# Performance work log

Hardware: AMD Instinct MI355X
Metric: run time of the kernel (lower is better)

Reference implementation:

```python
import jax, jax.numpy as jnp
import numpy as np

N = 20000        # nodes
E = 160000       # directed edges (before self loops)
NODE_DIM = 1287
HEADS = 4
C1, C2, C3 = 128, 256, 128
ACT_SLOPE = 0.15   # module's LeakyReLU between layers
GAT_SLOPE = 0.2    # PyG GATConv default negative_slope


def _gat_layer(x, src, dst, W, att_src, att_dst, bias, heads, out_dim, concat):
    # x: [N, in] ; W: [in, heads*out] ; att_*: [heads, out] ; bias: [heads*out] or [out]
    h = (x @ W).reshape(N, heads, out_dim)                      # [N, H, C]
    a_s = jnp.einsum('nhc,hc->nh', h, att_src)                  # [N, H]
    a_d = jnp.einsum('nhc,hc->nh', h, att_dst)                  # [N, H]
    e = jax.nn.leaky_relu(a_s[src] + a_d[dst], GAT_SLOPE)       # [Etot, H]
    # segment softmax over incoming edges of each dst node (self loops => no empty segments)
    m = jax.ops.segment_max(e, dst, num_segments=N)             # [N, H]
    w = jnp.exp(e - m[dst])
    den = jax.ops.segment_sum(w, dst, num_segments=N)           # [N, H]
    alpha = w / den[dst]                                        # [Etot, H]
    msg = h[src] * alpha[:, :, None]                            # [Etot, H, C]
    out = jax.ops.segment_sum(msg, dst, num_segments=N)         # [N, H, C]
    out = out.reshape(N, heads * out_dim) if concat else out.mean(axis=1)
    return out + bias


def setup_inputs() -> dict:
    key = jax.random.key(0)
    ks = jax.random.split(key, 22)
    s = 0.05
    x = jax.random.normal(ks[0], (N, NODE_DIM), jnp.float32)
    edge_index = jax.random.randint(ks[1], (2, E), 0, N, dtype=jnp.int64)
    inp = {
        'x': x, 'edge_index': edge_index,
        'W1': jax.random.normal(ks[2], (NODE_DIM, HEADS * C1), jnp.float32) * s,
        'as1': jax.random.normal(ks[3], (HEADS, C1), jnp.float32) * s,
        'ad1': jax.random.normal(ks[4], (HEADS, C1), jnp.float32) * s,
        'b1': jnp.zeros((HEADS * C1,), jnp.float32),
        'W2': jax.random.normal(ks[5], (HEADS * C1, HEADS * C2), jnp.float32) * s,
        'as2': jax.random.normal(ks[6], (HEADS, C2), jnp.float32) * s,
        'ad2': jax.random.normal(ks[7], (HEADS, C2), jnp.float32) * s,
        'b2': jnp.zeros((HEADS * C2,), jnp.float32),
        # conv3: 1024 -> 128, 1 head, no concat
        'W3': jax.random.normal(ks[8], (HEADS * C2, C3), jnp.float32) * s,
        'as3': jax.random.normal(ks[9], (1, C3), jnp.float32) * s,
        'ad3': jax.random.normal(ks[10], (1, C3), jnp.float32) * s,
        'b3': jnp.zeros((C3,), jnp.float32),
        # pre_fc: 128 -> 16
        'pw': jax.random.normal(ks[11], (C3, 16), jnp.float32) * s,
        'pb': jnp.zeros((16,), jnp.float32),
        # fc fallback: Linear(16,32) -> LeakyReLU(0.15) -> Linear(32,2)
        'f1w': jax.random.normal(ks[12], (16, 32), jnp.float32) * s,
        'f1b': jnp.zeros((32,), jnp.float32),
        'f2w': jax.random.normal(ks[13], (32, 2), jnp.float32) * s,
        'f2b': jnp.zeros((2,), jnp.float32),
    }
    return inp


def reference(x, edge_index, W1, as1, ad1, b1, W2, as2, ad2, b2,
              W3, as3, ad3, b3, pw, pb, f1w, f1b, f2w, f2b):
    loop = jnp.arange(N, dtype=edge_index.dtype)
    src = jnp.concatenate([edge_index[0], loop])   # PyG add_self_loops=True
    dst = jnp.concatenate([edge_index[1], loop])
    h = _gat_layer(x, src, dst, W1, as1, ad1, b1, HEADS, C1, True)
    h = jax.nn.leaky_relu(h, ACT_SLOPE)            # dropout = identity (eval)
    h = _gat_layer(h, src, dst, W2, as2, ad2, b2, HEADS, C2, True)
    h = jax.nn.leaky_relu(h, ACT_SLOPE)
    h = _gat_layer(h, src, dst, W3, as3, ad3, b3, 1, C3, False)
    h = jax.nn.leaky_relu(h, ACT_SLOPE)
    h = h @ pw + pb                                 # pre_fc (128 -> 16)
    h = jax.nn.leaky_relu(h @ f1w + f1b, ACT_SLOPE)
    return h @ f2w + f2b                            # [N, 2] logits
```

## Files before the change

### kernel.cpp

```cpp
#include <hip/hip_runtime.h>
#include <hip/hip_bf16.h>
#include <cstdint>
#include <cstddef>

#define LRELU(x, s) ((x) > 0.f ? (x) : (s) * (x))

typedef __attribute__((ext_vector_type(8))) short bf16x8;
typedef __attribute__((ext_vector_type(4))) float f32x4;

__device__ __forceinline__ float bflo(uint v) { return __uint_as_float(v << 16); }
__device__ __forceinline__ float bfhi(uint v) { return __uint_as_float(v & 0xffff0000u); }
__device__ __forceinline__ ushort f2bf(float f) {
  const uint u = __float_as_uint(f);
  return (ushort)((u + 0x7fffu + ((u >> 16) & 1u)) >> 16);
}
__device__ __forceinline__ float rl_f(float x, int j) {
  return __uint_as_float(__builtin_amdgcn_readlane(__float_as_uint(x), j));
}

__device__ __forceinline__ void async16(const ushort* g, ushort* l) {
  __builtin_amdgcn_global_load_lds(
      (const __attribute__((address_space(1))) unsigned int*)g,
      (__attribute__((address_space(3))) unsigned int*)l, 16, 0, 0);
}

#define WAITCNT_VM(n) (0xF70 | (n))

__global__ __launch_bounds__(256) void prep_all(
    const float* __restrict__ x, ushort* __restrict__ xb,
    const float* __restrict__ W1, ushort* __restrict__ W1t,
    const float* __restrict__ W2, ushort* __restrict__ W2t,
    const float* __restrict__ W3, ushort* __restrict__ W3t,
    const int* __restrict__ edst, int* __restrict__ deg, int E,
    int N, int K1, int K1p, int nA, int nB, int nC, int nD) {
  __shared__ float tile[32][33];
  const int tid = threadIdx.x;
  int b = blockIdx.x;
  if (b < nA) {
    const int P8 = K1p >> 3;
    const long long idx = (long long)b * 256 + tid;
    if (idx < (long long)N * P8) {
      const int r = (int)(idx / P8);
      const int c = ((int)(idx - (long long)r * P8)) << 3;
      const float* p = x + (size_t)r * K1 + c;
      float v[8];
      if (c + 7 < K1) {
        const float4 a = *(const float4*)p;
        const float4 bq = *(const float4*)(p + 4);
        v[0] = a.x; v[1] = a.y; v[2] = a.z; v[3] = a.w;
        v[4] = bq.x; v[5] = bq.y; v[6] = bq.z; v[7] = bq.w;
      } else {
#pragma unroll
        for (int j = 0; j < 8; j++) v[j] = (c + j < K1) ? p[j] : 0.f;
      }
      uint4 o;
      o.x = (uint)f2bf(v[0]) | ((uint)f2bf(v[1]) << 16);
      o.y = (uint)f2bf(v[2]) | ((uint)f2bf(v[3]) << 16);
      o.z = (uint)f2bf(v[4]) | ((uint)f2bf(v[5]) << 16);
      o.w = (uint)f2bf(v[6]) | ((uint)f2bf(v[7]) << 16);
      *(uint4*)(xb + (size_t)r * K1p + c) = o;
    }
    return;
  }
  b -= nA;
  if (b < nB + nC + nD) {
    const float* W; ushort* Wt; int K, Nn, Kp, tilesK;
    if (b < nB)           { W = W1; Wt = W1t; K = K1;   Nn = 512;  Kp = K1p;  tilesK = K1p / 32; }
    else if (b < nB + nC) { b -= nB; W = W2; Wt = W2t; K = 512;  Nn = 1024; Kp = 512;  tilesK = 16; }
    else                  { b -= nB + nC; W = W3; Wt = W3t; K = 1024; Nn = 128; Kp = 1024; tilesK = 32; }
    const int kt = (b % tilesK) * 32;
    const int nt = (b / tilesK) * 32;
    const int tx = tid & 31, ty = tid >> 5;
    for (int r = ty; r < 32; r += 8) {
      const int k = kt + r, nn = nt + tx;
      tile[r][tx] = (k < K && nn < Nn) ? W[(size_t)k * Nn + nn] : 0.f;
    }
    __syncthreads();
    for (int r = ty; r < 32; r += 8) {
      const int nn = nt + r, k = kt + tx;
      if (nn < Nn && k < Kp) Wt[(size_t)nn * Kp + k] = f2bf(tile[tx][r]);
    }
    return;
  }
  b -= nB + nC + nD;
  {
    const int t = b * 256 + tid;
    if (t < E) atomicAdd(&deg[edst[t]], 1);
  }
}

template <int TM, int TAG, bool BUF3>
__global__ __launch_bounds__(256) void gemm_bf16(
    const ushort* __restrict__ A, const ushort* __restrict__ Bt, ushort* __restrict__ C,
    int M, int N, int Kp, int gemmBlocks,
    const int* __restrict__ esrc, const int* __restrict__ edst, int E, int Etot,
    int* __restrict__ cursor, int* __restrict__ csr_src) {
  constexpr int MI = TM / 32;
  constexpr int LPG = (TM == 128) ? 4 : 3;
  constexpr int NBUF = BUF3 ? 3 : 2;
  __shared__ ushort sA[NBUF * TM * 32];
  __shared__ ushort sB[NBUF * 128 * 32];
  const int tid = threadIdx.x;
  const int wave = tid >> 6;
  const int lane = tid & 63;

  if (blockIdx.x >= gemmBlocks) {
    const int t = (blockIdx.x - gemmBlocks) * 256 + tid;
    if (t >= Etot) return;
    int s, d;
    if (t < E) { s = esrc[t]; d = edst[t]; } else { s = t - E; d = s; }
    const int pos = atomicAdd(&cursor[d], 1);
    csr_src[pos] = s;
    return;
  }

  const int tilesN = N >> 7;
  const int nwg = gemmBlocks;
  const int q8 = nwg >> 3, r8 = nwg & 7;
  const int xcd = blockIdx.x & 7;
  const int lid = blockIdx.x >> 3;
  const int wg = (xcd < r8 ? xcd * (q8 + 1) : r8 * (q8 + 1) + (xcd - r8) * q8) + lid;
  const int bx = wg % tilesN;
  const int by = wg / tilesN;
  const int wrow = (wave >> 1) * (TM / 2);
  const int wcol = (wave & 1) * 64;
  const int quad = lane >> 4;
  const int ml = lane & 15;

  const int seg = (((lane & 3) ^ ((lane >> 3) & 3)) * 8);
  const int rB0 = wave * 32 + (lane >> 2);
  const int gB0 = bx * 128 + rB0;
  const ushort* pB0 = Bt + (size_t)gB0 * Kp + seg;
  const ushort* pB1 = Bt + (size_t)(gB0 + 16) * Kp + seg;
  ushort* lB0 = &sB[(wave * 32) * 32];
  ushort* lB1 = &sB[(wave * 32 + 16) * 32];
  const ushort *pA0, *pA1;
  ushort *lA0, *lA1;
  if constexpr (TM == 128) {
    const int r0 = wave * 32 + (lane >> 2);
    pA0 = A + (size_t)min(by * TM + r0, M - 1) * Kp + seg;
    pA1 = A + (size_t)min(by * TM + r0 + 16, M - 1) * Kp + seg;
    lA0 = &sA[(wave * 32) * 32];
    lA1 = &sA[(wave * 32 + 16) * 32];
  } else {
    const int r0 = wave * 16 + (lane >> 2);
    pA0 = A + (size_t)min(by * TM + r0, M - 1) * Kp + seg;
    pA1 = nullptr;
    lA0 = &sA[(wave * 16) * 32];
    lA1 = nullptr;
  }

  const int nIter = Kp >> 5;
  auto issue = [&](int it, int p) {
    const int k0 = it << 5;
    const int oa = p * TM * 32;
    const int ob_ = p * 128 * 32;
    async16(pA0 + k0, lA0 + oa);
    if constexpr (TM == 128) async16(pA1 + k0, lA1 + oa);
    async16(pB0 + k0, lB0 + ob_);
    async16(pB1 + k0, lB1 + ob_);
  };

  f32x4 acc[MI][4];
#pragma unroll
  for (int mi = 0; mi < MI; mi++)
#pragma unroll
    for (int ni = 0; ni < 4; ni++)
#pragma unroll
      for (int e = 0; e < 4; e++) acc[mi][ni][e] = 0.f;

  const int rq = (quad ^ ((ml >> 1) & 3)) * 8;

  issue(0, 0);
  if (nIter > 1) issue(1, 1);
  int b = 0;
  for (int it = 0; it < nIter; ++it) {
    if (it + 1 < nIter) __builtin_amdgcn_s_waitcnt(WAITCNT_VM(LPG));
    else __builtin_amdgcn_s_waitcnt(WAITCNT_VM(0));
    __builtin_amdgcn_s_barrier();
    if constexpr (BUF3) {
      if (it + 2 < nIter) {
        const int b2 = (b + 2 >= 3) ? b - 1 : b + 2;
        issue(it + 2, b2);
      }
    }
    const ushort* bA = &sA[b * TM * 32];
    const ushort* bB = &sB[b * 128 * 32];
    bf16x8 af[MI], bfr[4];
#pragma unroll
    for (int mi = 0; mi < MI; mi++)
      af[mi] = *(const bf16x8*)&bA[(wrow + mi * 16 + ml) * 32 + rq];
#pragma unroll
    for (int ni = 0; ni < 4; ni++)
      bfr[ni] = *(const bf16x8*)&bB[(wcol + ni * 16 + ml) * 32 + rq];
#pragma unroll
    for (int mi = 0; mi < MI; mi++)
#pragma unroll
      for (int ni = 0; ni < 4; ni++)
        acc[mi][ni] = __builtin_amdgcn_mfma_f32_16x16x32_bf16(af[mi], bfr[ni], acc[mi][ni], 0, 0, 0);
    if constexpr (!BUF3) {
      if (it + 2 < nIter) {
        __builtin_amdgcn_s_barrier();
        issue(it + 2, b);
      }
      b ^= 1;
    } else {
      b = (b + 1 == 3) ? 0 : b + 1;
    }
  }

#pragma unroll
  for (int mi = 0; mi < MI; mi++) {
#pragma unroll
    for (int r = 0; r < 4; r++) {
      const int row = by * TM + wrow + mi * 16 + quad * 4 + r;
      if (row < M) {
#pragma unroll
        for (int ni = 0; ni < 4; ni++) {
          const int col = bx * 128 + wcol + ni * 16 + ml;
          C[(size_t)row * N + col] = f2bf(acc[mi][ni][r]);
        }
      }
    }
  }
}

template <int H, int C>
__global__ __launch_bounds__(256) void att_dots(
    const ushort* __restrict__ hb, const float* __restrict__ AS,
    const float* __restrict__ AD, float* __restrict__ asb, float* __restrict__ adb,
    int Nn) {
  constexpr int HC = H * C;
  constexpr int EPL = HC / 64;
  constexpr int S = C / EPL;
  const int n = blockIdx.x * 4 + (threadIdx.x >> 6);
  const int lane = threadIdx.x & 63;
  if (n >= Nn) return;
  const int head = lane / S;
  const int cbase = (lane % S) * EPL;
  const ushort* row = hb + (size_t)n * HC + lane * EPL;
  const float* as_h = AS + head * C;
  const float* ad_h = AD + head * C;
  float ps = 0.f, pd = 0.f;
#pragma unroll
  for (int j = 0; j < EPL; j += 2) {
    const uint v = *(const uint*)(row + j);
    const float lo = bflo(v), hi = bfhi(v);
    ps += lo * as_h[cbase + j] + hi * as_h[cbase + j + 1];
    pd += lo * ad_h[cbase + j] + hi * ad_h[cbase + j + 1];
  }
#pragma unroll
  for (int off = 1; off < S; off <<= 1) {
    ps += __shfl_xor(ps, off);
    pd += __shfl_xor(pd, off);
  }
  if ((lane % S) == 0) {
    asb[n * H + head] = ps;
    adb[n * H + head] = pd;
  }
}

__global__ __launch_bounds__(1024) void scan_kernel(const int* __restrict__ deg,
                                                    int* __restrict__ rowptr,
                                                    int* __restrict__ cursor, int n) {
  __shared__ int swsum[16];
  __shared__ int carry_s;
  const int t = threadIdx.x;
  const int wv = t >> 6, lane = t & 63;
  if (t == 0) carry_s = 0;
  __syncthreads();
  for (int base = 0; base < n; base += 1024) {
    const int i = base + t;
    const int v = (i < n) ? (deg[i] + 1) : 0;
    int sc = v;
#pragma unroll
    for (int off = 1; off < 64; off <<= 1) {
      const int u = __shfl_up(sc, off);
      if (lane >= off) sc += u;
    }
    if (lane == 63) swsum[wv] = sc;
    __syncthreads();
    if (t < 16) {
      int x = swsum[t];
#pragma unroll
      for (int off = 1; off < 16; off <<= 1) {
        const int u = __shfl_up(x, off);
        if (t >= off) x += u;
      }
      swsum[t] = x;
    }
    __syncthreads();
    const int incl = sc + (wv == 0 ? 0 : swsum[wv - 1]) + carry_s;
    if (i < n) { rowptr[i + 1] = incl; cursor[i] = incl - v; }
    if (base == 0 && t == 0) rowptr[0] = 0;
    __syncthreads();
    if (t == 0) carry_s += swsum[15];
    __syncthreads();
  }
}

template <int H, int C>
__global__ __launch_bounds__(256) void gat_agg_wave(
    const ushort* __restrict__ hb, const int* __restrict__ rowptr,
    const int* __restrict__ csr_src, const float* __restrict__ a_s,
    const float* __restrict__ a_d, const float* __restrict__ bias,
    ushort* __restrict__ outb, float act_slope, int Nn) {
  constexpr int HC = H * C;
  constexpr int NU = HC / 2;
  constexpr int UPT = NU / 256;
  constexpr int GRP = (UPT == 2) ? 4 : 8;
  const int n = blockIdx.x * 4 + (threadIdx.x >> 6);
  const int lane = threadIdx.x & 63;
  if (n >= Nn) return;
  float ad_n[H];
#pragma unroll
  for (int h = 0; h < H; h++) ad_n[h] = a_d[n * H + h];
  const int start = rowptr[n], end = rowptr[n + 1];
  f32x4 acc[UPT][2];
#pragma unroll
  for (int q = 0; q < UPT; q++)
#pragma unroll
    for (int u = 0; u < 2; u++)
#pragma unroll
      for (int e = 0; e < 4; e++) acc[q][u][e] = 0.f;
  float den[H];
#pragma unroll
  for (int h = 0; h < H; h++) den[h] = 0.f;

  for (int base = start; base < end; base += 64) {
    const int cnt = min(64, end - base);
    int s = 0;
    float w[H];
#pragma unroll
    for (int h = 0; h < H; h++) w[h] = 0.f;
    if (lane < cnt) {
      s = csr_src[base + lane];
      float asv[H];
      if constexpr (H == 4) {
        const float4 t4 = *(const float4*)(a_s + s * 4);
        asv[0] = t4.x; asv[1] = t4.y; asv[2] = t4.z; asv[3] = t4.w;
      } else {
        asv[0] = a_s[s];
      }
#pragma unroll
      for (int h = 0; h < H; h++) {
        float lg = asv[h] + ad_n[h];
        lg = LRELU(lg, 0.2f);
        w[h] = __expf(lg);
        den[h] += w[h];
      }
    }
    const int cntg = cnt & ~(GRP - 1);
    int j = 0;
    for (; j < cntg; j += GRP) {
      uint4 v[GRP][UPT];
#pragma unroll
      for (int g = 0; g < GRP; g++) {
        const int sj = __builtin_amdgcn_readlane(s, j + g);
        const uint4* hp = (const uint4*)(hb + (size_t)sj * HC);
#pragma unroll
        for (int q = 0; q < UPT; q++) v[g][q] = hp[q * 64 + lane];
      }
#pragma unroll
      for (int g = 0; g < GRP; g++) {
        float wj[H];
#pragma unroll
        for (int h = 0; h < H; h++) wj[h] = rl_f(w[h], j + g);
#pragma unroll
        for (int q = 0; q < UPT; q++) {
          const int e0 = q * 512 + 8 * lane;
          const float wq = wj[e0 / C];
          acc[q][0][0] += wq * bflo(v[g][q].x);
          acc[q][0][1] += wq * bfhi(v[g][q].x);
          acc[q][0][2] += wq * bflo(v[g][q].y);
          acc[q][0][3] += wq * bfhi(v[g][q].y);
          acc[q][1][0] += wq * bflo(v[g][q].z);
          acc[q][1][1] += wq * bfhi(v[g][q].z);
          acc[q][1][2] += wq * bflo(v[g][q].w);
          acc[q][1][3] += wq * bfhi(v[g][q].w);
        }
      }
    }
    for (; j < cnt; j++) {
      const int sj = __builtin_amdgcn_readlane(s, j);
      float wj[H];
#pragma unroll
      for (int h = 0; h < H; h++) wj[h] = rl_f(w[h], j);
      const uint4* hp = (const uint4*)(hb + (size_t)sj * HC);
#pragma unroll
      for (int q = 0; q < UPT; q++) {
        const int e0 = q * 512 + 8 * lane;
        const uint4 v = hp[q * 64 + lane];
        const float wq = wj[e0 / C];
        acc[q][0][0] += wq * bflo(v.x);
        acc[q][0][1] += wq * bfhi(v.x);
        acc[q][0][2] += wq * bflo(v.y);
        acc[q][0][3] += wq * bfhi(v.y);
        acc[q][1][0] += wq * bflo(v.z);
        acc[q][1][1] += wq * bfhi(v.z);
        acc[q][1][2] += wq * bflo(v.w);
        acc[q][1][3] += wq * bfhi(v.w);
      }
    }
  }
#pragma unroll
  for (int h = 0; h < H; h++) {
#pragma unroll
    for (int off = 1; off < 64; off <<= 1) den[h] += __shfl_xor(den[h], off);
    den[h] = 1.f / den[h];
  }
#pragma unroll
  for (int q = 0; q < UPT; q++) {
    const int e0 = q * 512 + 8 * lane;
    const float iv = den[e0 / C];
    const float4 ba = *(const float4*)(bias + e0);
    const float4 bb = *(const float4*)(bias + e0 + 4);
    const float o0 = LRELU(acc[q][0][0] * iv + ba.x, act_slope);
    const float o1 = LRELU(acc[q][0][1] * iv + ba.y, act_slope);
    const float o2 = LRELU(acc[q][0][2] * iv + ba.z, act_slope);
    const float o3 = LRELU(acc[q][0][3] * iv + ba.w, act_slope);
    const float o4 = LRELU(acc[q][1][0] * iv + bb.x, act_slope);
    const float o5 = LRELU(acc[q][1][1] * iv + bb.y, act_slope);
    const float o6 = LRELU(acc[q][1][2] * iv + bb.z, act_slope);
    const float o7 = LRELU(acc[q][1][3] * iv + bb.w, act_slope);
    uint4 o;
    o.x = (uint)f2bf(o0) | ((uint)f2bf(o1) << 16);
    o.y = (uint)f2bf(o2) | ((uint)f2bf(o3) << 16);
    o.z = (uint)f2bf(o4) | ((uint)f2bf(o5) << 16);
    o.w = (uint)f2bf(o6) | ((uint)f2bf(o7) << 16);
    ((uint4*)outb)[(size_t)n * (NU / 4) + q * 64 + lane] = o;
  }
}

__global__ __launch_bounds__(256) void gat_agg3_mlp(
    const ushort* __restrict__ hb, const int* __restrict__ rowptr,
    const int* __restrict__ csr_src, const float* __restrict__ a_s,
    const float* __restrict__ a_d, const float* __restrict__ b3,
    const float* __restrict__ pw, const float* __restrict__ pb,
    const float* __restrict__ f1w, const float* __restrict__ f1b,
    const float* __restrict__ f2w, const float* __restrict__ f2b,
    float* __restrict__ out, int Nn) {
  __shared__ float sx[4][128];
  __shared__ float s1[4][16];
  __shared__ float s2[4][32];
  const int w = threadIdx.x >> 6;
  const int lane = threadIdx.x & 63;
  const int n = blockIdx.x * 4 + w;
  if (n >= Nn) return;
  const float ad_n = a_d[n];
  const int start = rowptr[n], end = rowptr[n + 1];
  float2 acc = make_float2(0.f, 0.f);
  float den = 0.f;
  for (int base = start; base < end; base += 64) {
    const int cnt = min(64, end - base);
    int s = 0;
    float wv_ = 0.f;
    if (lane < cnt) {
      s = csr_src[base + lane];
      float lg = a_s[s] + ad_n;
      lg = LRELU(lg, 0.2f);
      wv_ = __expf(lg);
      den += wv_;
    }
    const int cntg = cnt & ~7;
    int j = 0;
    for (; j < cntg; j += 8) {
      uint v[8];
      float wj[8];
#pragma unroll
      for (int g = 0; g < 8; g++) {
        const int sj = __builtin_amdgcn_readlane(s, j + g);
        v[g] = ((const uint*)(hb + (size_t)sj * 128))[lane];
        wj[g] = rl_f(wv_, j + g);
      }
#pragma unroll
      for (int g = 0; g < 8; g++) {
        acc.x += wj[g] * bflo(v[g]);
        acc.y += wj[g] * bfhi(v[g]);
      }
    }
    for (; j < cnt; j++) {
      const int sj = __builtin_amdgcn_readlane(s, j);
      const float wj = rl_f(wv_, j);
      const uint v = ((const uint*)(hb + (size_t)sj * 128))[lane];
      acc.x += wj * bflo(v);
      acc.y += wj * bfhi(v);
    }
  }
#pragma unroll
  for (int off = 1; off < 64; off <<= 1) den += __shfl_xor(den, off);
  const float iv = 1.f / den;
  sx[w][2 * lane]     = LRELU(acc.x * iv + b3[2 * lane], 0.15f);
  sx[w][2 * lane + 1] = LRELU(acc.y * iv + b3[2 * lane + 1], 0.15f);
  {
    const int o = lane & 15, p = lane >> 4;
    float a = 0.f;
#pragma unroll
    for (int c = 0; c < 32; c++) a += sx[w][p * 32 + c] * pw[(p * 32 + c) * 16 + o];
    a += __shfl_xor(a, 16);
    a += __shfl_xor(a, 32);
    if (lane < 16) s1[w][o] = a + pb[o];
  }
  {
    const int o = lane & 31, p = lane >> 5;
    float a = 0.f;
#pragma unroll
    for (int c = 0; c < 8; c++) a += s1[w][p * 8 + c] * f1w[(p * 8 + c) * 32 + o];
    a += __shfl_xor(a, 32);
    if (lane < 32) s2[w][o] = LRELU(a + f1b[o], 0.15f);
  }
  {
    const int o = lane & 1, p = lane >> 1;
    float a = s2[w][p] * f2w[p * 2 + o];
    a += __shfl_xor(a, 2);
    a += __shfl_xor(a, 4);
    a += __shfl_xor(a, 8);
    a += __shfl_xor(a, 16);
    a += __shfl_xor(a, 32);
    if (lane < 2) out[(size_t)n * 2 + o] = a + f2b[o];
  }
}

extern "C" void kernel_launch(void* const* d_in, const int* in_sizes, int n_in,
                              void* d_out, int out_size, void* d_ws, size_t ws_size,
                              hipStream_t stream) {
  const float* x   = (const float*)d_in[0];
  const int* ei    = (const int*)d_in[1];
  const float* W1  = (const float*)d_in[2];
  const float* as1 = (const float*)d_in[3];
  const float* ad1 = (const float*)d_in[4];
  const float* b1  = (const float*)d_in[5];
  const float* W2  = (const float*)d_in[6];
  const float* as2 = (const float*)d_in[7];
  const float* ad2 = (const float*)d_in[8];
  const float* b2  = (const float*)d_in[9];
  const float* W3  = (const float*)d_in[10];
  const float* as3 = (const float*)d_in[11];
  const float* ad3 = (const float*)d_in[12];
  const float* b3  = (const float*)d_in[13];
  const float* pw  = (const float*)d_in[14];
  const float* pb  = (const float*)d_in[15];
  const float* f1w = (const float*)d_in[16];
  const float* f1b = (const float*)d_in[17];
  const float* f2w = (const float*)d_in[18];
  const float* f2b = (const float*)d_in[19];
  float* out = (float*)d_out;

  const int N = in_sizes[0] / 1287;
  const int E = in_sizes[1] / 2;
  const int Etot = E + N;
  const int* esrc = ei;
  const int* edst = ei + E;
  const int K1 = 1287, K1p = 1312;

  char* ws = (char*)d_ws;
  size_t off = 0;
  auto alloc = [&](size_t bytes) -> void* {
    void* p = ws + off;
    off = (off + bytes + 255) & ~(size_t)255;
    return p;
  };
  ushort* hb  = (ushort*)alloc((size_t)N * 1024 * 2);
  ushort* ob  = (ushort*)alloc((size_t)N * 1024 * 2);
  ushort* xb  = (ushort*)alloc((size_t)N * K1p * 2);
  ushort* W1t = (ushort*)alloc((size_t)512 * K1p * 2);
  ushort* W2t = (ushort*)alloc((size_t)1024 * 512 * 2);
  ushort* W3t = (ushort*)alloc((size_t)128 * 1024 * 2);
  float* av   = (float*)alloc((size_t)N * 8 * sizeof(float));
  int* deg    = (int*)alloc((size_t)N * sizeof(int));
  int* rowptr = (int*)alloc((size_t)(N + 1) * sizeof(int));
  int* cursor = (int*)alloc((size_t)N * sizeof(int));
  int* csr    = (int*)alloc((size_t)Etot * sizeof(int));
  float* asb = av;
  float* adb = av + (size_t)N * 4;

  hipMemsetAsync(deg, 0, (size_t)N * sizeof(int), stream);
  const int nA = (int)(((long long)N * (K1p / 8) + 255) / 256);
  const int nB = (K1p / 32) * (512 / 32);
  const int nC = (512 / 32) * (1024 / 32);
  const int nD = (1024 / 32) * (128 / 32);
  const int nCnt = (E + 255) / 256;
  prep_all<<<nA + nB + nC + nD + nCnt, 256, 0, stream>>>(
      x, xb, W1, W1t, W2, W2t, W3, W3t,
      edst, deg, E, N, K1, K1p, nA, nB, nC, nD);

  scan_kernel<<<1, 1024, 0, stream>>>(deg, rowptr, cursor, N);

  const int tilesM = (N + 127) / 128;
  const int tilesM64 = (N + 63) / 64;
  const int nodeBlocks = (N + 3) / 4;
  const int scatB = (Etot + 255) / 256;

  {
    const int g = tilesM * 4;
    gemm_bf16<128, 1, true><<<g + scatB, 256, 0, stream>>>(
        xb, W1t, hb, N, 512, K1p, g, esrc, edst, E, Etot, cursor, csr);
    att_dots<4, 128><<<nodeBlocks, 256, 0, stream>>>(hb, as1, ad1, asb, adb, N);
    gat_agg_wave<4, 128><<<nodeBlocks, 256, 0, stream>>>(hb, rowptr, csr, asb, adb,
                                                         b1, ob, 0.15f, N);
  }
  {
    const int g = tilesM * 8;
    gemm_bf16<128, 2, false><<<g, 256, 0, stream>>>(
        ob, W2t, hb, N, 1024, 512, g, nullptr, nullptr, 0, 0, nullptr, nullptr);
    att_dots<4, 256><<<nodeBlocks, 256, 0, stream>>>(hb, as2, ad2, asb, adb, N);
    gat_agg_wave<4, 256><<<nodeBlocks, 256, 0, stream>>>(hb, rowptr, csr, asb, adb,
                                                         b2, ob, 0.15f, N);
  }
  {
    gemm_bf16<64, 3, true><<<tilesM64, 256, 0, stream>>>(
        ob, W3t, hb, N, 128, 1024, tilesM64, nullptr, nullptr, 0, 0, nullptr, nullptr);
    att_dots<1, 128><<<nodeBlocks, 256, 0, stream>>>(hb, as3, ad3, asb, adb, N);
    gat_agg3_mlp<<<nodeBlocks, 256, 0, stream>>>(hb, rowptr, csr, asb, adb, b3,
                                                 pw, pb, f1w, f1b, f2w, f2b, out, N);
  }
}
```

Before: 440.6 us.

## Fold degree scan into GEMM1 launch and move CSR scatter into att_dots

Removes the standalone single-block scan kernel launch. The prefix scan now runs as one extra 256-thread block in the layer-1 GEMM grid, and the CSR scatter moves from the GEMM grid into the att_dots launch. This hides the serial scan behind GEMM work and saves a launch. The cost is a slower scan, since a 256-thread block runs about 80 serial iterations, which may extend the GEMM kernel's tail.

```diff
diff --git a/kernel.cpp b/kernel.cpp
--- a/kernel.cpp
+++ b/kernel.cpp
@@ -25,6 +25,41 @@
 }
 
 #define WAITCNT_VM(n) (0xF70 | (n))
+
+__device__ void scan_block256(const int* __restrict__ deg, int* __restrict__ rowptr,
+                              int* __restrict__ cursor, int n) {
+  __shared__ int swsum[4];
+  __shared__ int carry_s;
+  const int t = threadIdx.x;
+  const int wv = t >> 6, lane = t & 63;
+  if (t == 0) carry_s = 0;
+  __syncthreads();
+  for (int base = 0; base < n; base += 256) {
+    const int i = base + t;
+    const int v = (i < n) ? (deg[i] + 1) : 0;
+    int sc = v;
+#pragma unroll
+    for (int off = 1; off < 64; off <<= 1) {
+      const int u = __shfl_up(sc, off);
+      if (lane >= off) sc += u;
+    }
+    if (lane == 63) swsum[wv] = sc;
+    __syncthreads();
+    if (t == 0) {
+      int a = swsum[0];
+      a += swsum[1]; swsum[1] = a;
+      a += swsum[2]; swsum[2] = a;
+      a += swsum[3]; swsum[3] = a;
+    }
+    __syncthreads();
+    const int incl = sc + (wv == 0 ? 0 : swsum[wv - 1]) + carry_s;
+    if (i < n) { rowptr[i + 1] = incl; cursor[i] = incl - v; }
+    if (base == 0 && t == 0) rowptr[0] = 0;
+    __syncthreads();
+    if (t == 0) carry_s += swsum[3];
+    __syncthreads();
+  }
+}
 
 __global__ __launch_bounds__(256) void prep_all(
     const float* __restrict__ x, ushort* __restrict__ xb,
@@ -93,8 +128,8 @@
 __global__ __launch_bounds__(256) void gemm_bf16(
     const ushort* __restrict__ A, const ushort* __restrict__ Bt, ushort* __restrict__ C,
     int M, int N, int Kp, int gemmBlocks,
-    const int* __restrict__ esrc, const int* __restrict__ edst, int E, int Etot,
-    int* __restrict__ cursor, int* __restrict__ csr_src) {
+    const int* __restrict__ deg, int* __restrict__ rowptr, int* __restrict__ cursor,
+    int scanN) {
   constexpr int MI = TM / 32;
   constexpr int LPG = (TM == 128) ? 4 : 3;
   constexpr int NBUF = BUF3 ? 3 : 2;
@@ -105,12 +140,7 @@
   const int lane = tid & 63;
 
   if (blockIdx.x >= gemmBlocks) {
-    const int t = (blockIdx.x - gemmBlocks) * 256 + tid;
-    if (t >= Etot) return;
-    int s, d;
-    if (t < E) { s = esrc[t]; d = edst[t]; } else { s = t - E; d = s; }
-    const int pos = atomicAdd(&cursor[d], 1);
-    csr_src[pos] = s;
+    scan_block256(deg, rowptr, cursor, scanN);
     return;
   }
 
@@ -229,12 +259,23 @@
 __global__ __launch_bounds__(256) void att_dots(
     const ushort* __restrict__ hb, const float* __restrict__ AS,
     const float* __restrict__ AD, float* __restrict__ asb, float* __restrict__ adb,
-    int Nn) {
+    int Nn, int dotsBlocks,
+    const int* __restrict__ esrc, const int* __restrict__ edst, int E, int Etot,
+    int* __restrict__ cursor, int* __restrict__ csr_src) {
   constexpr int HC = H * C;
   constexpr int EPL = HC / 64;
   constexpr int S = C / EPL;
+  const int lane = threadIdx.x & 63;
+  if (blockIdx.x >= dotsBlocks) {
+    const int t = (blockIdx.x - dotsBlocks) * 256 + threadIdx.x;
+    if (t >= Etot) return;
+    int s, d;
+    if (t < E) { s = esrc[t]; d = edst[t]; } else { s = t - E; d = s; }
+    const int pos = atomicAdd(&cursor[d], 1);
+    csr_src[pos] = s;
+    return;
+  }
   const int n = blockIdx.x * 4 + (threadIdx.x >> 6);
-  const int lane = threadIdx.x & 63;
   if (n >= Nn) return;
   const int head = lane / S;
   const int cbase = (lane % S) * EPL;
@@ -257,45 +298,6 @@
   if ((lane % S) == 0) {
     asb[n * H + head] = ps;
     adb[n * H + head] = pd;
-  }
-}
-
-__global__ __launch_bounds__(1024) void scan_kernel(const int* __restrict__ deg,
-                                                    int* __restrict__ rowptr,
-                                                    int* __restrict__ cursor, int n) {
-  __shared__ int swsum[16];
-  __shared__ int carry_s;
-  const int t = threadIdx.x;
-  const int wv = t >> 6, lane = t & 63;
-  if (t == 0) carry_s = 0;
-  __syncthreads();
-  for (int base = 0; base < n; base += 1024) {
-    const int i = base + t;
-    const int v = (i < n) ? (deg[i] + 1) : 0;
-    int sc = v;
-#pragma unroll
-    for (int off = 1; off < 64; off <<= 1) {
-      const int u = __shfl_up(sc, off);
-      if (lane >= off) sc += u;
-    }
-    if (lane == 63) swsum[wv] = sc;
-    __syncthreads();
-    if (t < 16) {
-      int x = swsum[t];
-#pragma unroll
-      for (int off = 1; off < 16; off <<= 1) {
-        const int u = __shfl_up(x, off);
-        if (t >= off) x += u;
-      }
-      swsum[t] = x;
-    }
-    __syncthreads();
-    const int incl = sc + (wv == 0 ? 0 : swsum[wv - 1]) + carry_s;
-    if (i < n) { rowptr[i + 1] = incl; cursor[i] = incl - v; }
-    if (base == 0 && t == 0) rowptr[0] = 0;
-    __syncthreads();
-    if (t == 0) carry_s += swsum[15];
-    __syncthreads();
   }
 }
 
@@ -584,8 +586,6 @@
       x, xb, W1, W1t, W2, W2t, W3, W3t,
       edst, deg, E, N, K1, K1p, nA, nB, nC, nD);
 
-  scan_kernel<<<1, 1024, 0, stream>>>(deg, rowptr, cursor, N);
-
   const int tilesM = (N + 127) / 128;
   const int tilesM64 = (N + 63) / 64;
   const int nodeBlocks = (N + 3) / 4;
@@ -593,24 +593,27 @@
 
   {
     const int g = tilesM * 4;
-    gemm_bf16<128, 1, true><<<g + scatB, 256, 0, stream>>>(
-        xb, W1t, hb, N, 512, K1p, g, esrc, edst, E, Etot, cursor, csr);
-    att_dots<4, 128><<<nodeBlocks, 256, 0, stream>>>(hb, as1, ad1, asb, adb, N);
+    gemm_bf16<128, 1, true><<<g + 1, 256, 0, stream>>>(
+        xb, W1t, hb, N, 512, K1p, g, deg, rowptr, cursor, N);
+    att_dots<4, 128><<<nodeBlocks + scatB, 256, 0, stream>>>(
+        hb, as1, ad1, asb, adb, N, nodeBlocks, esrc, edst, E, Etot, cursor, csr);
     gat_agg_wave<4, 128><<<nodeBlocks, 256, 0, stream>>>(hb, rowptr, csr, asb, adb,
                                                          b1, ob, 0.15f, N);
   }
   {
     const int g = tilesM * 8;
     gemm_bf16<128, 2, false><<<g, 256, 0, stream>>>(
-        ob, W2t, hb, N, 1024, 512, g, nullptr, nullptr, 0, 0, nullptr, nullptr);
-    att_dots<4, 256><<<nodeBlocks, 256, 0, stream>>>(hb, as2, ad2, asb, adb, N);
+        ob, W2t, hb, N, 1024, 512, g, nullptr, nullptr, nullptr, 0);
+    att_dots<4, 256><<<nodeBlocks, 256, 0, stream>>>(
+        hb, as2, ad2, asb, adb, N, nodeBlocks, nullptr, nullptr, 0, 0, nullptr, nullptr);
     gat_agg_wave<4, 256><<<nodeBlocks, 256, 0, stream>>>(hb, rowptr, csr, asb, adb,
                                                          b2, ob, 0.15f, N);
   }
   {
     gemm_bf16<64, 3, true><<<tilesM64, 256, 0, stream>>>(
-        ob, W3t, hb, N, 128, 1024, tilesM64, nullptr, nullptr, 0, 0, nullptr, nullptr);
-    att_dots<1, 128><<<nodeBlocks, 256, 0, stream>>>(hb, as3, ad3, asb, adb, N);
+        ob, W3t, hb, N, 128, 1024, tilesM64, nullptr, nullptr, nullptr, 0);
+    att_dots<1, 128><<<nodeBlocks, 256, 0, stream>>>(
+        hb, as3, ad3, asb, adb, N, nodeBlocks, nullptr, nullptr, 0, 0, nullptr, nullptr);
     gat_agg3_mlp<<<nodeBlocks, 256, 0, stream>>>(hb, rowptr, csr, asb, adb, b3,
                                                  pw, pb, f1w, f1b, f2w, f2b, out, N);
   }
```

After: 455.9 us. 3.5% more time.
